# Kernel tuning notes

Measured on AMD Instinct MI355X. Metric: run time of the kernel, lower is better.

## Reference

```python
import jax, jax.numpy as jnp
import numpy as np
from math import sqrt

BATCH = 32
NUM_CLASSES = 81   # incl. background (class 0 skipped)
MAX_DET = 200      # max_output / per-class NMS candidate cap
IOU_T = 0.5        # criteria in decode_batch_with_nms_trace
CONF_T = 0.05      # score mask threshold


def make_dboxes():
    """Replicates dboxes_R34_coco([1200,1200]) -> (15130, 4) xywh, clipped to [0,1]."""
    fig = 1200
    feat = [50, 25, 13, 7, 3, 3]
    scales = [int(s * fig / 300) for s in [21, 45, 99, 153, 207, 261, 315]]
    ars = [[2], [2, 3], [2, 3], [2, 3], [2], [2]]
    boxes = []
    for idx, f in enumerate(feat):
        sk1 = scales[idx] / fig
        sk2 = scales[idx + 1] / fig
        sk3 = sqrt(sk1 * sk2)
        sizes = [(sk1, sk1), (sk3, sk3)]
        for a in ars[idx]:
            w, h = sk1 * sqrt(a), sk1 / sqrt(a)
            sizes += [(w, h), (h, w)]
        fk = fig // (fig // f)
        for (w, h) in sizes:
            for i in range(f):
                for j in range(f):
                    boxes.append(((j + 0.5) / fk, (i + 0.5) / fk, w, h))
    return np.clip(np.asarray(boxes, np.float32), 0.0, 1.0)


def setup_inputs() -> dict:
    key = jax.random.key(0)
    k1, k2 = jax.random.split(key)
    db = make_dboxes()                      # (15130, 4)
    N = db.shape[0]
    return {
        "bboxes_in": jax.random.normal(k1, (BATCH, 4, N), jnp.float32),
        "scores_in": jax.random.normal(k2, (BATCH, NUM_CLASSES, N), jnp.float32),
        "scale_xy": jnp.full((1,), 0.1, jnp.float32),
        "scale_wh": jnp.full((1,), 0.2, jnp.float32),
        "dboxes_xywh": jnp.asarray(db)[None],  # (1, N, 4)
    }


def _scale_back(bboxes_in, scores_in, scale_xy, scale_wh, dboxes_xywh):
    bb = jnp.transpose(bboxes_in, (0, 2, 1))          # (B, N, 4)
    sc = jnp.transpose(scores_in, (0, 2, 1))          # (B, N, L)
    d_xy, d_wh = dboxes_xywh[..., :2], dboxes_xywh[..., 2:]
    xy = bb[..., :2] * scale_xy * d_wh + d_xy
    wh = jnp.exp(bb[..., 2:] * scale_wh) * d_wh
    ltrb = jnp.concatenate([xy - 0.5 * wh, xy + 0.5 * wh], axis=-1)
    return ltrb, jax.nn.softmax(sc, axis=-1)


def _pairwise_iou(a, b):
    lt = jnp.maximum(a[:, None, :2], b[None, :, :2])
    rb = jnp.minimum(a[:, None, 2:], b[None, :, 2:])
    wh = jnp.clip(rb - lt, 0.0)
    inter = wh[..., 0] * wh[..., 1]
    area_a = (a[:, 2] - a[:, 0]) * (a[:, 3] - a[:, 1])
    area_b = (b[:, 2] - b[:, 0]) * (b[:, 3] - b[:, 1])
    return inter / (area_a[:, None] + area_b[None, :] - inter)


def _nms_one_class(boxes, cls_scores):
    """boxes (N,4), cls_scores (N,) -> (MAX_DET,4), (MAX_DET,) with suppressed = -1."""
    s = jnp.where(cls_scores > CONF_T, cls_scores, -1.0)   # mask score > 0.05
    top_s, idx = jax.lax.top_k(s, MAX_DET)                 # descending topk
    b = boxes[idx]
    iou = _pairwise_iou(b, b)                              # (K, K)
    valid = top_s > CONF_T

    def body(i, keep):  # greedy NMS over score-sorted candidates
        sup = (iou[i] > IOU_T) & keep[i] & (jnp.arange(MAX_DET) > i)
        return keep & ~sup

    keep = jax.lax.stop_gradient(jax.lax.fori_loop(0, MAX_DET, body, valid))
    return b, jnp.where(keep, top_s, -1.0)


def _decode(bboxes_in, scores_in, scale_xy, scale_wh, dboxes_xywh):
    boxes, probs = _scale_back(bboxes_in, scores_in, scale_xy, scale_wh, dboxes_xywh)
    cls_scores = jnp.transpose(probs[..., 1:], (0, 2, 1))   # (B, C=80, N); skip bg
    B, C = cls_scores.shape[0], cls_scores.shape[1]
    per_class = jax.vmap(_nms_one_class, in_axes=(None, 0))
    kb, ks = jax.vmap(per_class, in_axes=(0, 0))(boxes, cls_scores)  # (B,C,K,4),(B,C,K)
    labels = jnp.broadcast_to(
        jnp.arange(1, C + 1, dtype=jnp.int32)[:, None], (C, MAX_DET)).reshape(-1)
    kb = kb.reshape(B, C * MAX_DET, 4)
    ks = ks.reshape(B, C * MAX_DET)
    top_s, top_i = jax.lax.top_k(ks, MAX_DET)               # global top-200
    fb = jnp.take_along_axis(kb, top_i[..., None], axis=1)  # (B, 200, 4)
    fl = labels[top_i]                                      # (B, 200)
    valid = top_s > CONF_T
    return (fb * valid[..., None].astype(fb.dtype),
            jnp.where(valid, fl, 0),
            jnp.where(valid, top_s, 0.0))


def reference(bboxes_in, scores_in, scale_xy, scale_wh, dboxes_xywh):
    return _decode(bboxes_in, scores_in, scale_xy, scale_wh, dboxes_xywh)
```

## Files before the change

kernel.cpp:

```cpp
#include <hip/hip_runtime.h>
#include <stdint.h>

#define NPRIOR   15130
#define BATCH    32
#define NCLS     81
#define NCLS_OUT 80
#define NDET     200
#define CONF_T   0.05f
#define IOU_T    0.5f
#define CAND_CAP 1024
#define NGRP     5
#define GRP      16

__global__ __launch_bounds__(256) void zero_counters(unsigned int* __restrict__ counters, int n) {
    int i = blockIdx.x * 256 + threadIdx.x;
    if (i < n) counters[i] = 0u;
}

__global__ __launch_bounds__(256) void decode_softmax_scatter(
    const float* __restrict__ bboxes,
    const float* __restrict__ scores,
    const float* __restrict__ scale_xy_p,
    const float* __restrict__ scale_wh_p,
    const float* __restrict__ dboxes,
    float* __restrict__ boxes_ltrb,
    unsigned int* __restrict__ counters,
    unsigned long long* __restrict__ cand_g)
{
    int b = blockIdx.y;
    int n = blockIdx.x * 256 + threadIdx.x;
    if (n >= NPRIOR) return;

    float sx = scale_xy_p[0], sw = scale_wh_p[0];
    const float* bb = bboxes + (size_t)b * 4 * NPRIOR + n;
    float bx = bb[0];
    float by = bb[NPRIOR];
    float bw = bb[2 * NPRIOR];
    float bh = bb[3 * NPRIOR];
    float dx = dboxes[n * 4 + 0], dy = dboxes[n * 4 + 1];
    float dw = dboxes[n * 4 + 2], dh = dboxes[n * 4 + 3];
    float x = __fadd_rn(__fmul_rn(__fmul_rn(bx, sx), dw), dx);
    float y = __fadd_rn(__fmul_rn(__fmul_rn(by, sx), dh), dy);
    float w = __fmul_rn(expf(__fmul_rn(bw, sw)), dw);
    float h = __fmul_rn(expf(__fmul_rn(bh, sw)), dh);
    float hw = __fmul_rn(0.5f, w), hh = __fmul_rn(0.5f, h);
    float4 box;
    box.x = __fsub_rn(x, hw);
    box.y = __fsub_rn(y, hh);
    box.z = __fadd_rn(x, hw);
    box.w = __fadd_rn(y, hh);
    ((float4*)boxes_ltrb)[(size_t)b * NPRIOR + n] = box;

    const float* sc = scores + (size_t)b * NCLS * NPRIOR + n;
    float v[NCLS];
    float mx = -INFINITY;
#pragma unroll
    for (int c = 0; c < NCLS; ++c) {
        v[c] = sc[(size_t)c * NPRIOR];
        mx = fmaxf(mx, v[c]);
    }
    float sum = 0.f;
#pragma unroll
    for (int c = 0; c < NCLS; ++c) {
        v[c] = expf(__fsub_rn(v[c], mx));
        sum = __fadd_rn(sum, v[c]);
    }

    unsigned int invn = 0xFFFFFFFFu - (unsigned int)n;
#pragma unroll
    for (int c = 1; c < NCLS; ++c) {
        float p = __fdiv_rn(v[c], sum);
        if (p > CONF_T) {
            unsigned int idx = (unsigned int)b * NCLS_OUT + (unsigned int)(c - 1);
            unsigned int pos = atomicAdd(&counters[idx], 1u);
            if (pos < CAND_CAP) {
                cand_g[(size_t)idx * CAND_CAP + pos] =
                    ((unsigned long long)__float_as_uint(p) << 32) | (unsigned long long)invn;
            }
        }
    }
}

__device__ inline void bitonic_desc(unsigned long long* keys, int P, int tid) {
    for (int k = 2; k <= P; k <<= 1) {
        for (int j = k >> 1; j > 0; j >>= 1) {
            for (int i = tid; i < P; i += 256) {
                int l = i ^ j;
                if (l > i) {
                    unsigned long long a = keys[i], b = keys[l];
                    bool desc = ((i & k) == 0);
                    if (desc ? (a < b) : (a > b)) {
                        keys[i] = b;
                        keys[l] = a;
                    }
                }
            }
            __syncthreads();
        }
    }
}

__global__ __launch_bounds__(256) void nms_class(
    const unsigned int* __restrict__ counters,
    const unsigned long long* __restrict__ cand_g,
    const float* __restrict__ boxes_ltrb,
    float* __restrict__ cls_scores,
    float* __restrict__ cls_boxes)
{
    __shared__ unsigned long long cand[CAND_CAP];
    __shared__ float sbox[NDET][4];
    __shared__ float sscore[NDET];
    __shared__ unsigned long long rowm[NDET][4];
    __shared__ unsigned long long keepw[4];

    int tid = threadIdx.x;
    int b = blockIdx.y;
    int bc = b * NCLS_OUT + blockIdx.x;

    unsigned int cntu = counters[bc];
    int cnt = (cntu > CAND_CAP) ? CAND_CAP : (int)cntu;

    int P = 256;
    while (P < cnt) P <<= 1;

    for (int i = tid; i < P; i += 256)
        cand[i] = (i < cnt) ? cand_g[(size_t)bc * CAND_CAP + i] : 0ull;
    __syncthreads();

    bitonic_desc(cand, P, tid);

    int m = cnt < NDET ? cnt : NDET;
    if (tid < m) {
        unsigned long long key = cand[tid];
        unsigned int n = 0xFFFFFFFFu - (unsigned int)(key & 0xFFFFFFFFull);
        sscore[tid] = __uint_as_float((unsigned int)(key >> 32));
        float4 bx = ((const float4*)boxes_ltrb)[(size_t)b * NPRIOR + n];
        sbox[tid][0] = bx.x;
        sbox[tid][1] = bx.y;
        sbox[tid][2] = bx.z;
        sbox[tid][3] = bx.w;
    }
    __syncthreads();

    if (tid < m) {
        float l0 = sbox[tid][0], t0 = sbox[tid][1], r0 = sbox[tid][2], b0 = sbox[tid][3];
        float area0 = __fmul_rn(__fsub_rn(r0, l0), __fsub_rn(b0, t0));
        unsigned long long w0 = 0, w1 = 0, w2 = 0, w3 = 0;
        for (int j = tid + 1; j < m; ++j) {
            float lj = sbox[j][0], tj = sbox[j][1], rj = sbox[j][2], bj = sbox[j][3];
            float ltx = fmaxf(l0, lj), lty = fmaxf(t0, tj);
            float rbx = fminf(r0, rj), rby = fminf(b0, bj);
            float iw = fmaxf(__fsub_rn(rbx, ltx), 0.f);
            float ih = fmaxf(__fsub_rn(rby, lty), 0.f);
            float inter = __fmul_rn(iw, ih);
            float areaj = __fmul_rn(__fsub_rn(rj, lj), __fsub_rn(bj, tj));
            float den = __fsub_rn(__fadd_rn(area0, areaj), inter);
            float iou = __fdiv_rn(inter, den);
            if (iou > IOU_T) {
                if (j < 64) w0 |= 1ull << j;
                else if (j < 128) w1 |= 1ull << (j - 64);
                else if (j < 192) w2 |= 1ull << (j - 128);
                else w3 |= 1ull << (j - 192);
            }
        }
        rowm[tid][0] = w0;
        rowm[tid][1] = w1;
        rowm[tid][2] = w2;
        rowm[tid][3] = w3;
    }
    __syncthreads();

    if (tid == 0) {
        auto maskf = [](int t) -> unsigned long long {
            if (t <= 0) return 0ull;
            if (t >= 64) return ~0ull;
            return (1ull << t) - 1ull;
        };
        unsigned long long k0 = maskf(m), k1 = maskf(m - 64), k2 = maskf(m - 128), k3 = maskf(m - 192);
        for (int i = 0; i < m; ++i) {
            unsigned long long cur = (i < 64) ? k0 : (i < 128) ? k1 : (i < 192) ? k2 : k3;
            if ((cur >> (i & 63)) & 1ull) {
                k0 &= ~rowm[i][0];
                k1 &= ~rowm[i][1];
                k2 &= ~rowm[i][2];
                k3 &= ~rowm[i][3];
            }
        }
        keepw[0] = k0; keepw[1] = k1; keepw[2] = k2; keepw[3] = k3;
    }
    __syncthreads();

    if (tid < NDET) {
        float s = -1.0f;
        if (tid < m && ((keepw[tid >> 6] >> (tid & 63)) & 1ull)) s = sscore[tid];
        cls_scores[(size_t)bc * NDET + tid] = s;
        if (tid < m) {
            float4 bx;
            bx.x = sbox[tid][0]; bx.y = sbox[tid][1];
            bx.z = sbox[tid][2]; bx.w = sbox[tid][3];
            ((float4*)cls_boxes)[(size_t)bc * NDET + tid] = bx;
        }
    }
}

__global__ __launch_bounds__(256) void topk_group(
    const float* __restrict__ cls_scores,
    unsigned long long* __restrict__ grp_keys)
{
    __shared__ unsigned long long keys[4096];
    __shared__ unsigned int cnt_s;

    int tid = threadIdx.x;
    int g = blockIdx.x, b = blockIdx.y;
    if (tid == 0) cnt_s = 0;
    __syncthreads();

    int base_e = g * GRP * NDET;
    const float* sp = cls_scores + (size_t)b * NCLS_OUT * NDET + base_e;
    for (int i = tid; i < GRP * NDET; i += 256) {
        float s = sp[i];
        if (s > CONF_T) {
            unsigned int pos = atomicAdd(&cnt_s, 1u);
            unsigned int e = (unsigned int)(base_e + i);
            keys[pos] = ((unsigned long long)__float_as_uint(s) << 32) |
                        (unsigned long long)(0xFFFFFFFFu - e);
        }
    }
    __syncthreads();
    int cnt = (int)cnt_s;
    int P = 256;
    while (P < cnt) P <<= 1;
    for (int i = tid; i < P; i += 256)
        if (i >= cnt) keys[i] = 0ull;
    __syncthreads();

    bitonic_desc(keys, P, tid);

    if (tid < NDET)
        grp_keys[((size_t)b * NGRP + g) * NDET + tid] = (tid < cnt) ? keys[tid] : 0ull;
}

__global__ __launch_bounds__(256) void final_topk(
    const unsigned long long* __restrict__ grp_keys,
    const float* __restrict__ cls_boxes,
    float* __restrict__ out)
{
    __shared__ unsigned long long keys[1024];
    __shared__ unsigned int cnt_s;

    int tid = threadIdx.x, b = blockIdx.x;
    if (tid == 0) cnt_s = 0;
    __syncthreads();

    for (int i = tid; i < NGRP * NDET; i += 256) {
        unsigned long long k = grp_keys[(size_t)b * NGRP * NDET + i];
        if (k != 0ull) keys[atomicAdd(&cnt_s, 1u)] = k;
    }
    __syncthreads();
    int cnt = (int)cnt_s;
    int P = 256;
    while (P < cnt) P <<= 1;
    for (int i = tid; i < P; i += 256)
        if (i >= cnt) keys[i] = 0ull;
    __syncthreads();

    bitonic_desc(keys, P, tid);

    if (tid < NDET) {
        float4 bx = make_float4(0.f, 0.f, 0.f, 0.f);
        float lab = 0.f, sc = 0.f;
        if (tid < cnt) {
            unsigned long long k = keys[tid];
            unsigned int e = 0xFFFFFFFFu - (unsigned int)(k & 0xFFFFFFFFull);
            sc = __uint_as_float((unsigned int)(k >> 32));
            unsigned int c0 = e / NDET;
            bx = ((const float4*)cls_boxes)[(size_t)b * NCLS_OUT * NDET + e];
            lab = (float)(c0 + 1);
        }
        float* fb = out;
        float* fl = out + (size_t)BATCH * NDET * 4;
        float* fs = fl + (size_t)BATCH * NDET;
        ((float4*)fb)[b * NDET + tid] = bx;
        fl[b * NDET + tid] = lab;
        fs[b * NDET + tid] = sc;
    }
}

extern "C" void kernel_launch(void* const* d_in, const int* in_sizes, int n_in,
                              void* d_out, int out_size, void* d_ws, size_t ws_size,
                              hipStream_t stream) {
    const float* bboxes = (const float*)d_in[0];
    const float* scores = (const float*)d_in[1];
    const float* sxy    = (const float*)d_in[2];
    const float* swh    = (const float*)d_in[3];
    const float* dbx    = (const float*)d_in[4];
    float* out = (float*)d_out;

    char* ws = (char*)d_ws;
    size_t off = 0;
    auto alloc = [&](size_t bytes) -> char* {
        char* p = ws + off;
        off += (bytes + 255) & ~(size_t)255;
        return p;
    };
    float* boxes_ltrb            = (float*)alloc((size_t)BATCH * NPRIOR * 4 * 4);
    unsigned int* counters       = (unsigned int*)alloc((size_t)BATCH * NCLS_OUT * 4);
    unsigned long long* cand_g   = (unsigned long long*)alloc((size_t)BATCH * NCLS_OUT * CAND_CAP * 8);
    float* cls_scores            = (float*)alloc((size_t)BATCH * NCLS_OUT * NDET * 4);
    float* cls_boxes             = (float*)alloc((size_t)BATCH * NCLS_OUT * NDET * 4 * 4);
    unsigned long long* grp_keys = (unsigned long long*)alloc((size_t)BATCH * NGRP * NDET * 8);

    int ncounters = BATCH * NCLS_OUT;
    zero_counters<<<(ncounters + 255) / 256, 256, 0, stream>>>(counters, ncounters);

    dim3 gridA((NPRIOR + 255) / 256, BATCH);
    decode_softmax_scatter<<<gridA, 256, 0, stream>>>(
        bboxes, scores, sxy, swh, dbx, boxes_ltrb, counters, cand_g);

    dim3 gridB(NCLS_OUT, BATCH);
    nms_class<<<gridB, 256, 0, stream>>>(counters, cand_g, boxes_ltrb, cls_scores, cls_boxes);

    dim3 gridC1(NGRP, BATCH);
    topk_group<<<gridC1, 256, 0, stream>>>(cls_scores, grp_keys);

    final_topk<<<BATCH, 256, 0, stream>>>(grp_keys, cls_boxes, out);
}
```

Baseline: 800.1 us.

## Stage softmax scores through LDS and split box decode across thread halves

The decode/softmax kernel now handles 128 priors per block. All 256 threads cooperatively load the 81-class score tile into shared memory with float2 loads, while the upper half of the block computes box decoding. After a barrier, the lower half computes the softmax from LDS rather than holding 81 values in registers. A cheap pre-check (e > CONF_T) skips the division for most classes, which is valid because sum >= 1. The aim is lower register pressure and better load throughput, at the cost of idle threads during the softmax phase and 41KB of LDS per block.

New measurement: 1.010 ms. 26.3% more time.

```diff
diff --git a/kernel.cpp b/kernel.cpp
--- a/kernel.cpp
+++ b/kernel.cpp
@@ -11,6 +11,7 @@
 #define CAND_CAP 1024
 #define NGRP     5
 #define GRP      16
+#define PRB      128
 
 __global__ __launch_bounds__(256) void zero_counters(unsigned int* __restrict__ counters, int n) {
     int i = blockIdx.x * 256 + threadIdx.x;
@@ -27,55 +28,82 @@
     unsigned int* __restrict__ counters,
     unsigned long long* __restrict__ cand_g)
 {
+    __shared__ float lds_sc[NCLS * PRB];
+
+    int tid = threadIdx.x;
     int b = blockIdx.y;
-    int n = blockIdx.x * 256 + threadIdx.x;
-    if (n >= NPRIOR) return;
-
-    float sx = scale_xy_p[0], sw = scale_wh_p[0];
-    const float* bb = bboxes + (size_t)b * 4 * NPRIOR + n;
-    float bx = bb[0];
-    float by = bb[NPRIOR];
-    float bw = bb[2 * NPRIOR];
-    float bh = bb[3 * NPRIOR];
-    float dx = dboxes[n * 4 + 0], dy = dboxes[n * 4 + 1];
-    float dw = dboxes[n * 4 + 2], dh = dboxes[n * 4 + 3];
-    float x = __fadd_rn(__fmul_rn(__fmul_rn(bx, sx), dw), dx);
-    float y = __fadd_rn(__fmul_rn(__fmul_rn(by, sx), dh), dy);
-    float w = __fmul_rn(expf(__fmul_rn(bw, sw)), dw);
-    float h = __fmul_rn(expf(__fmul_rn(bh, sw)), dh);
-    float hw = __fmul_rn(0.5f, w), hh = __fmul_rn(0.5f, h);
-    float4 box;
-    box.x = __fsub_rn(x, hw);
-    box.y = __fsub_rn(y, hh);
-    box.z = __fadd_rn(x, hw);
-    box.w = __fadd_rn(y, hh);
-    ((float4*)boxes_ltrb)[(size_t)b * NPRIOR + n] = box;
-
-    const float* sc = scores + (size_t)b * NCLS * NPRIOR + n;
-    float v[NCLS];
-    float mx = -INFINITY;
-#pragma unroll
-    for (int c = 0; c < NCLS; ++c) {
-        v[c] = sc[(size_t)c * NPRIOR];
-        mx = fmaxf(mx, v[c]);
-    }
-    float sum = 0.f;
-#pragma unroll
-    for (int c = 0; c < NCLS; ++c) {
-        v[c] = expf(__fsub_rn(v[c], mx));
-        sum = __fadd_rn(sum, v[c]);
-    }
-
-    unsigned int invn = 0xFFFFFFFFu - (unsigned int)n;
-#pragma unroll
-    for (int c = 1; c < NCLS; ++c) {
-        float p = __fdiv_rn(v[c], sum);
-        if (p > CONF_T) {
-            unsigned int idx = (unsigned int)b * NCLS_OUT + (unsigned int)(c - 1);
-            unsigned int pos = atomicAdd(&counters[idx], 1u);
-            if (pos < CAND_CAP) {
-                cand_g[(size_t)idx * CAND_CAP + pos] =
-                    ((unsigned long long)__float_as_uint(p) << 32) | (unsigned long long)invn;
+    int base = blockIdx.x * PRB;
+    int nvalid = NPRIOR - base;
+    if (nvalid > PRB) nvalid = PRB;
+
+    {
+        const float* sb = scores + (size_t)b * NCLS * NPRIOR + base;
+        const int nf2 = NCLS * (PRB / 2);
+        for (int q = tid; q < nf2; q += 256) {
+            int c = q >> 6;
+            int p = (q & 63) << 1;
+            if (p < nvalid) {
+                float2 val = *(const float2*)(sb + (size_t)c * NPRIOR + p);
+                *(float2*)&lds_sc[c * PRB + p] = val;
+            }
+        }
+    }
+
+    if (tid >= PRB) {
+        int t = tid - PRB;
+        if (t < nvalid) {
+            int n = base + t;
+            float sx = scale_xy_p[0], sw = scale_wh_p[0];
+            const float* bb = bboxes + (size_t)b * 4 * NPRIOR + n;
+            float bx = bb[0];
+            float by = bb[NPRIOR];
+            float bw = bb[2 * NPRIOR];
+            float bh = bb[3 * NPRIOR];
+            float dx = dboxes[n * 4 + 0], dy = dboxes[n * 4 + 1];
+            float dw = dboxes[n * 4 + 2], dh = dboxes[n * 4 + 3];
+            float x = __fadd_rn(__fmul_rn(__fmul_rn(bx, sx), dw), dx);
+            float y = __fadd_rn(__fmul_rn(__fmul_rn(by, sx), dh), dy);
+            float w = __fmul_rn(expf(__fmul_rn(bw, sw)), dw);
+            float h = __fmul_rn(expf(__fmul_rn(bh, sw)), dh);
+            float hw = __fmul_rn(0.5f, w), hh = __fmul_rn(0.5f, h);
+            float4 box;
+            box.x = __fsub_rn(x, hw);
+            box.y = __fsub_rn(y, hh);
+            box.z = __fadd_rn(x, hw);
+            box.w = __fadd_rn(y, hh);
+            ((float4*)boxes_ltrb)[(size_t)b * NPRIOR + n] = box;
+        }
+    }
+
+    __syncthreads();
+
+    if (tid < PRB && tid < nvalid) {
+        int n = base + tid;
+
+        float mx = -INFINITY;
+        for (int c = 0; c < NCLS; ++c)
+            mx = fmaxf(mx, lds_sc[c * PRB + tid]);
+
+        float sum = 0.f;
+        for (int c = 0; c < NCLS; ++c) {
+            float e = expf(__fsub_rn(lds_sc[c * PRB + tid], mx));
+            sum = __fadd_rn(sum, e);
+            lds_sc[c * PRB + tid] = e;
+        }
+
+        unsigned int invn = 0xFFFFFFFFu - (unsigned int)n;
+        for (int c = 1; c < NCLS; ++c) {
+            float e = lds_sc[c * PRB + tid];
+            if (e > CONF_T) {
+                float p = __fdiv_rn(e, sum);
+                if (p > CONF_T) {
+                    unsigned int idx = (unsigned int)b * NCLS_OUT + (unsigned int)(c - 1);
+                    unsigned int pos = atomicAdd(&counters[idx], 1u);
+                    if (pos < CAND_CAP) {
+                        cand_g[(size_t)idx * CAND_CAP + pos] =
+                            ((unsigned long long)__float_as_uint(p) << 32) | (unsigned long long)invn;
+                    }
+                }
             }
         }
     }
@@ -313,7 +341,7 @@
     int ncounters = BATCH * NCLS_OUT;
     zero_counters<<<(ncounters + 255) / 256, 256, 0, stream>>>(counters, ncounters);
 
-    dim3 gridA((NPRIOR + 255) / 256, BATCH);
+    dim3 gridA((NPRIOR + PRB - 1) / PRB, BATCH);
     decode_softmax_scatter<<<gridA, 256, 0, stream>>>(
         bboxes, scores, sxy, swh, dbx, boxes_ltrb, counters, cand_g);
 
```

## Split per-prior softmax across four lanes and prefilter before division

Applied to the files above, without the earlier changes.

The decode/softmax/scatter kernel now gives each prior four lanes, each holding about 20 of the 81 class logits instead of one thread holding all 81. The max is combined with xor shuffles, and the sum is passed from group to group so the original summation order is kept. Only one lane group decodes the box. Since the softmax denominator is at least 1, a cheap `e > CONF_T` test now skips the division for most classes. This cuts register pressure and raises parallelism, at the cost of narrower 64-byte coalesced loads per class row and extra shuffles.

Measured after the change: 978.4 us. 1.22x slower.

```diff
diff --git a/kernel.cpp b/kernel.cpp
--- a/kernel.cpp
+++ b/kernel.cpp
@@ -27,55 +27,92 @@
     unsigned int* __restrict__ counters,
     unsigned long long* __restrict__ cand_g)
 {
-    int b = blockIdx.y;
-    int n = blockIdx.x * 256 + threadIdx.x;
-    if (n >= NPRIOR) return;
-
-    float sx = scale_xy_p[0], sw = scale_wh_p[0];
-    const float* bb = bboxes + (size_t)b * 4 * NPRIOR + n;
-    float bx = bb[0];
-    float by = bb[NPRIOR];
-    float bw = bb[2 * NPRIOR];
-    float bh = bb[3 * NPRIOR];
-    float dx = dboxes[n * 4 + 0], dy = dboxes[n * 4 + 1];
-    float dw = dboxes[n * 4 + 2], dh = dboxes[n * 4 + 3];
-    float x = __fadd_rn(__fmul_rn(__fmul_rn(bx, sx), dw), dx);
-    float y = __fadd_rn(__fmul_rn(__fmul_rn(by, sx), dh), dy);
-    float w = __fmul_rn(expf(__fmul_rn(bw, sw)), dw);
-    float h = __fmul_rn(expf(__fmul_rn(bh, sw)), dh);
-    float hw = __fmul_rn(0.5f, w), hh = __fmul_rn(0.5f, h);
-    float4 box;
-    box.x = __fsub_rn(x, hw);
-    box.y = __fsub_rn(y, hh);
-    box.z = __fadd_rn(x, hw);
-    box.w = __fadd_rn(y, hh);
-    ((float4*)boxes_ltrb)[(size_t)b * NPRIOR + n] = box;
+    int tid  = threadIdx.x;
+    int b    = blockIdx.y;
+    int wave = tid >> 6;
+    int lane = tid & 63;
+    int slot = lane & 15;
+    int h    = lane >> 4;
+    int n    = blockIdx.x * 64 + wave * 16 + slot;
+    bool active = (n < NPRIOR);
+
+    const int c0  = (h == 0) ? 0 : (21 + (h - 1) * 20);
+    const int cnt = (h == 0) ? 21 : 20;
 
     const float* sc = scores + (size_t)b * NCLS * NPRIOR + n;
-    float v[NCLS];
+
+    float v[21];
+#pragma unroll
+    for (int k = 0; k < 21; ++k) v[k] = -INFINITY;
+    if (active) {
+#pragma unroll
+        for (int k = 0; k < 21; ++k)
+            if (k < cnt) v[k] = sc[(size_t)(c0 + k) * NPRIOR];
+    }
+
+    if (active && h == 3) {
+        float sx = scale_xy_p[0], sw = scale_wh_p[0];
+        const float* bb = bboxes + (size_t)b * 4 * NPRIOR + n;
+        float bx = bb[0];
+        float by = bb[NPRIOR];
+        float bw = bb[2 * NPRIOR];
+        float bh = bb[3 * NPRIOR];
+        float dx = dboxes[n * 4 + 0], dy = dboxes[n * 4 + 1];
+        float dw = dboxes[n * 4 + 2], dh = dboxes[n * 4 + 3];
+        float x = __fadd_rn(__fmul_rn(__fmul_rn(bx, sx), dw), dx);
+        float y = __fadd_rn(__fmul_rn(__fmul_rn(by, sx), dh), dy);
+        float w = __fmul_rn(expf(__fmul_rn(bw, sw)), dw);
+        float hh_ = __fmul_rn(expf(__fmul_rn(bh, sw)), dh);
+        float hw = __fmul_rn(0.5f, w), hhh = __fmul_rn(0.5f, hh_);
+        float4 box;
+        box.x = __fsub_rn(x, hw);
+        box.y = __fsub_rn(y, hhh);
+        box.z = __fadd_rn(x, hw);
+        box.w = __fadd_rn(y, hhh);
+        ((float4*)boxes_ltrb)[(size_t)b * NPRIOR + n] = box;
+    }
+
     float mx = -INFINITY;
 #pragma unroll
-    for (int c = 0; c < NCLS; ++c) {
-        v[c] = sc[(size_t)c * NPRIOR];
-        mx = fmaxf(mx, v[c]);
-    }
-    float sum = 0.f;
-#pragma unroll
-    for (int c = 0; c < NCLS; ++c) {
-        v[c] = expf(__fsub_rn(v[c], mx));
-        sum = __fadd_rn(sum, v[c]);
-    }
-
-    unsigned int invn = 0xFFFFFFFFu - (unsigned int)n;
-#pragma unroll
-    for (int c = 1; c < NCLS; ++c) {
-        float p = __fdiv_rn(v[c], sum);
-        if (p > CONF_T) {
-            unsigned int idx = (unsigned int)b * NCLS_OUT + (unsigned int)(c - 1);
-            unsigned int pos = atomicAdd(&counters[idx], 1u);
-            if (pos < CAND_CAP) {
-                cand_g[(size_t)idx * CAND_CAP + pos] =
-                    ((unsigned long long)__float_as_uint(p) << 32) | (unsigned long long)invn;
+    for (int k = 0; k < 21; ++k)
+        if (k < cnt) mx = fmaxf(mx, v[k]);
+    mx = fmaxf(mx, __shfl_xor(mx, 16, 64));
+    mx = fmaxf(mx, __shfl_xor(mx, 32, 64));
+
+#pragma unroll
+    for (int k = 0; k < 21; ++k)
+        v[k] = expf(__fsub_rn(v[k], mx));
+
+    float cum = 0.f;
+#pragma unroll
+    for (int s = 0; s < 4; ++s) {
+        if (h == s) {
+#pragma unroll
+            for (int k = 0; k < 21; ++k)
+                if (k < cnt) cum = __fadd_rn(cum, v[k]);
+        }
+        cum = __shfl(cum, slot + s * 16, 64);
+    }
+    float sum = cum;
+
+    if (active) {
+        unsigned int invn = 0xFFFFFFFFu - (unsigned int)n;
+#pragma unroll
+        for (int k = 0; k < 21; ++k) {
+            int c = c0 + k;
+            if (k < cnt && c >= 1) {
+                float e = v[k];
+                if (e > CONF_T) {
+                    float p = __fdiv_rn(e, sum);
+                    if (p > CONF_T) {
+                        unsigned int idx = (unsigned int)b * NCLS_OUT + (unsigned int)(c - 1);
+                        unsigned int pos = atomicAdd(&counters[idx], 1u);
+                        if (pos < CAND_CAP) {
+                            cand_g[(size_t)idx * CAND_CAP + pos] =
+                                ((unsigned long long)__float_as_uint(p) << 32) | (unsigned long long)invn;
+                        }
+                    }
+                }
             }
         }
     }
@@ -313,7 +350,7 @@
     int ncounters = BATCH * NCLS_OUT;
     zero_counters<<<(ncounters + 255) / 256, 256, 0, stream>>>(counters, ncounters);
 
-    dim3 gridA((NPRIOR + 255) / 256, BATCH);
+    dim3 gridA((NPRIOR + 63) / 64, BATCH);
     decode_softmax_scatter<<<gridA, 256, 0, stream>>>(
         bboxes, scores, sxy, swh, dbx, boxes_ltrb, counters, cand_g);
 
```

## Stage scores in LDS and split softmax across four lanes; parallelize NMS keep scan

Applied to the files above, without the earlier changes.

The decode/softmax kernel now handles 64 priors per block and stages the 81 class scores in shared memory with vectorized loads. Four lanes share each prior, each covering 20 classes, and combine max and sum through shuffles. A per-lane flag mask limits division and atomics to candidates that could pass the threshold. The serial NMS suppression loop now runs across four lanes, one per 64-bit keep word, with the next suppression row prefetched; this adds a shuffle on every iteration.

Measured after the change: 920.5 us. +15.0%, slower.

```diff
diff --git a/kernel.cpp b/kernel.cpp
--- a/kernel.cpp
+++ b/kernel.cpp
@@ -11,6 +11,8 @@
 #define CAND_CAP 1024
 #define NGRP     5
 #define GRP      16
+#define PPB      64
+#define ROWW     68
 
 __global__ __launch_bounds__(256) void zero_counters(unsigned int* __restrict__ counters, int n) {
     int i = blockIdx.x * 256 + threadIdx.x;
@@ -27,55 +29,118 @@
     unsigned int* __restrict__ counters,
     unsigned long long* __restrict__ cand_g)
 {
+    __shared__ float lds[NCLS * ROWW];
+
+    int tid = threadIdx.x;
     int b = blockIdx.y;
-    int n = blockIdx.x * 256 + threadIdx.x;
-    if (n >= NPRIOR) return;
-
-    float sx = scale_xy_p[0], sw = scale_wh_p[0];
-    const float* bb = bboxes + (size_t)b * 4 * NPRIOR + n;
-    float bx = bb[0];
-    float by = bb[NPRIOR];
-    float bw = bb[2 * NPRIOR];
-    float bh = bb[3 * NPRIOR];
-    float dx = dboxes[n * 4 + 0], dy = dboxes[n * 4 + 1];
-    float dw = dboxes[n * 4 + 2], dh = dboxes[n * 4 + 3];
-    float x = __fadd_rn(__fmul_rn(__fmul_rn(bx, sx), dw), dx);
-    float y = __fadd_rn(__fmul_rn(__fmul_rn(by, sx), dh), dy);
-    float w = __fmul_rn(expf(__fmul_rn(bw, sw)), dw);
-    float h = __fmul_rn(expf(__fmul_rn(bh, sw)), dh);
-    float hw = __fmul_rn(0.5f, w), hh = __fmul_rn(0.5f, h);
-    float4 box;
-    box.x = __fsub_rn(x, hw);
-    box.y = __fsub_rn(y, hh);
-    box.z = __fadd_rn(x, hw);
-    box.w = __fadd_rn(y, hh);
-    ((float4*)boxes_ltrb)[(size_t)b * NPRIOR + n] = box;
-
-    const float* sc = scores + (size_t)b * NCLS * NPRIOR + n;
-    float v[NCLS];
+    int base = blockIdx.x * PPB;
+    int nvalid = NPRIOR - base;
+    if (nvalid > PPB) nvalid = PPB;
+
+    const float* sb = scores + (size_t)b * NCLS * NPRIOR + base;
+
+    if (nvalid == PPB) {
+        for (int i = tid; i < NCLS * (PPB / 2); i += 256) {
+            int c = i >> 5, q = i & 31;
+            float2 v = *(const float2*)(sb + (size_t)c * NPRIOR + q * 2);
+            *(float2*)&lds[c * ROWW + q * 2] = v;
+        }
+    } else {
+        for (int i = tid; i < NCLS * PPB; i += 256) {
+            int c = i >> 6, w = i & 63;
+            lds[c * ROWW + w] = (w < nvalid) ? sb[(size_t)c * NPRIOR + w] : 0.0f;
+        }
+    }
+
+    int wave = tid >> 6, lane = tid & 63, slot = lane & 15, h = lane >> 4;
+    int sg = wave * 16 + slot;
+    int n = base + sg;
+    bool active = (sg < nvalid);
+    int cbase = h * 20;
+
+    if (h == 0 && active) {
+        float sx = scale_xy_p[0], sw = scale_wh_p[0];
+        const float* bb = bboxes + (size_t)b * 4 * NPRIOR + n;
+        float bx = bb[0];
+        float by = bb[NPRIOR];
+        float bw = bb[2 * NPRIOR];
+        float bh = bb[3 * NPRIOR];
+        float dx = dboxes[n * 4 + 0], dy = dboxes[n * 4 + 1];
+        float dw = dboxes[n * 4 + 2], dh = dboxes[n * 4 + 3];
+        float x = __fadd_rn(__fmul_rn(__fmul_rn(bx, sx), dw), dx);
+        float y = __fadd_rn(__fmul_rn(__fmul_rn(by, sx), dh), dy);
+        float w  = __fmul_rn(expf(__fmul_rn(bw, sw)), dw);
+        float hg = __fmul_rn(expf(__fmul_rn(bh, sw)), dh);
+        float hw = __fmul_rn(0.5f, w), hh2 = __fmul_rn(0.5f, hg);
+        float4 box;
+        box.x = __fsub_rn(x, hw);
+        box.y = __fsub_rn(y, hh2);
+        box.z = __fadd_rn(x, hw);
+        box.w = __fadd_rn(y, hh2);
+        ((float4*)boxes_ltrb)[(size_t)b * NPRIOR + n] = box;
+    }
+
+    __syncthreads();
+
+    const int rb = cbase * ROWW + sg;
+
     float mx = -INFINITY;
-#pragma unroll
-    for (int c = 0; c < NCLS; ++c) {
-        v[c] = sc[(size_t)c * NPRIOR];
-        mx = fmaxf(mx, v[c]);
-    }
-    float sum = 0.f;
-#pragma unroll
-    for (int c = 0; c < NCLS; ++c) {
-        v[c] = expf(__fsub_rn(v[c], mx));
-        sum = __fadd_rn(sum, v[c]);
-    }
-
-    unsigned int invn = 0xFFFFFFFFu - (unsigned int)n;
-#pragma unroll
-    for (int c = 1; c < NCLS; ++c) {
-        float p = __fdiv_rn(v[c], sum);
-        if (p > CONF_T) {
-            unsigned int idx = (unsigned int)b * NCLS_OUT + (unsigned int)(c - 1);
-            unsigned int pos = atomicAdd(&counters[idx], 1u);
-            if (pos < CAND_CAP) {
-                cand_g[(size_t)idx * CAND_CAP + pos] =
-                    ((unsigned long long)__float_as_uint(p) << 32) | (unsigned long long)invn;
+    if (h == 0) mx = fmaxf(mx, lds[sg]);
+#pragma unroll
+    for (int k = 1; k <= 20; ++k)
+        mx = fmaxf(mx, lds[rb + k * ROWW]);
+    mx = fmaxf(mx, __shfl_xor(mx, 16, 64));
+    mx = fmaxf(mx, __shfl_xor(mx, 32, 64));
+
+    unsigned int flags = 0;
+    if (h == 0) lds[sg] = expf(__fsub_rn(lds[sg], mx));
+#pragma unroll
+    for (int k = 1; k <= 20; ++k) {
+        float e = expf(__fsub_rn(lds[rb + k * ROWW], mx));
+        lds[rb + k * ROWW] = e;
+        if (e > CONF_T) flags |= (1u << k);
+    }
+
+    float cum = 0.f;
+    if (h == 0) {
+        cum = __fadd_rn(cum, lds[sg]);
+#pragma unroll
+        for (int k = 1; k <= 20; ++k) cum = __fadd_rn(cum, lds[rb + k * ROWW]);
+    }
+    cum = __shfl(cum, slot, 64);
+    if (h == 1) {
+#pragma unroll
+        for (int k = 1; k <= 20; ++k) cum = __fadd_rn(cum, lds[rb + k * ROWW]);
+    }
+    cum = __shfl(cum, 16 + slot, 64);
+    if (h == 2) {
+#pragma unroll
+        for (int k = 1; k <= 20; ++k) cum = __fadd_rn(cum, lds[rb + k * ROWW]);
+    }
+    cum = __shfl(cum, 32 + slot, 64);
+    if (h == 3) {
+#pragma unroll
+        for (int k = 1; k <= 20; ++k) cum = __fadd_rn(cum, lds[rb + k * ROWW]);
+    }
+    cum = __shfl(cum, 48 + slot, 64);
+    float sum = cum;
+
+    if (active && flags) {
+        unsigned int invn = 0xFFFFFFFFu - (unsigned int)n;
+        unsigned int f = flags;
+        while (f) {
+            int k = __ffs(f) - 1;
+            f &= f - 1;
+            float e = lds[rb + k * ROWW];
+            float p = __fdiv_rn(e, sum);
+            if (p > CONF_T) {
+                int c = cbase + k;
+                unsigned int idx = (unsigned int)b * NCLS_OUT + (unsigned int)(c - 1);
+                unsigned int pos = atomicAdd(&counters[idx], 1u);
+                if (pos < CAND_CAP) {
+                    cand_g[(size_t)idx * CAND_CAP + pos] =
+                        ((unsigned long long)__float_as_uint(p) << 32) | (unsigned long long)invn;
+                }
             }
         }
     }
@@ -170,23 +235,26 @@
     }
     __syncthreads();
 
-    if (tid == 0) {
+    if (tid < 64) {
+        int lw = tid & 3;
         auto maskf = [](int t) -> unsigned long long {
             if (t <= 0) return 0ull;
             if (t >= 64) return ~0ull;
             return (1ull << t) - 1ull;
         };
-        unsigned long long k0 = maskf(m), k1 = maskf(m - 64), k2 = maskf(m - 128), k3 = maskf(m - 192);
+        unsigned long long keep = 0ull;
+        if (tid < 4) keep = maskf(m - lw * 64);
+        unsigned long long nxt = 0ull;
+        if (tid < 4 && m > 0) nxt = rowm[0][lw];
         for (int i = 0; i < m; ++i) {
-            unsigned long long cur = (i < 64) ? k0 : (i < 128) ? k1 : (i < 192) ? k2 : k3;
-            if ((cur >> (i & 63)) & 1ull) {
-                k0 &= ~rowm[i][0];
-                k1 &= ~rowm[i][1];
-                k2 &= ~rowm[i][2];
-                k3 &= ~rowm[i][3];
-            }
-        }
-        keepw[0] = k0; keepw[1] = k1; keepw[2] = k2; keepw[3] = k3;
+            int ow = i >> 6;
+            int bit = (int)((keep >> (i & 63)) & 1ull);
+            bit = __shfl(bit, ow, 64);
+            unsigned long long cur = nxt;
+            if (tid < 4 && i + 1 < m) nxt = rowm[i + 1][lw];
+            if (bit) keep &= ~cur;
+        }
+        if (tid < 4) keepw[lw] = keep;
     }
     __syncthreads();
 
@@ -313,7 +381,7 @@
     int ncounters = BATCH * NCLS_OUT;
     zero_counters<<<(ncounters + 255) / 256, 256, 0, stream>>>(counters, ncounters);
 
-    dim3 gridA((NPRIOR + 255) / 256, BATCH);
+    dim3 gridA((NPRIOR + PPB - 1) / PPB, BATCH);
     decode_softmax_scatter<<<gridA, 256, 0, stream>>>(
         bboxes, scores, sxy, swh, dbx, boxes_ltrb, counters, cand_g);
 
```
